# Optimization experiments

Measured on AMD Instinct MI355X. Metric: run time of the kernel, lower is better.

Reference implementation:

```python
import jax, jax.numpy as jnp
import numpy as np

DIM_V = 768
DIM_T = 768
HIDDEN = 256
MAX_KEEP = 96


def setup_inputs() -> dict:
    key = jax.random.key(0)
    k1, k2, k3, k4, k5 = jax.random.split(key, 5)
    B, N, S = 64, 1024, 64
    dense_visual = jax.random.normal(k1, (B, N, DIM_V), dtype=jnp.float32)
    text_embedding = jax.random.normal(k2, (B, S, DIM_T), dtype=jnp.float32)
    din = DIM_V + DIM_T
    # Linear params (stored as [in, out] for x @ W)
    W1 = jax.random.normal(k3, (din, HIDDEN), dtype=jnp.float32) / np.sqrt(din)
    b1 = jnp.zeros((HIDDEN,), dtype=jnp.float32)
    W2 = jax.random.normal(k4, (HIDDEN, 1), dtype=jnp.float32) / np.sqrt(HIDDEN)
    b2 = jnp.zeros((1,), dtype=jnp.float32)
    register_token = jax.random.normal(k5, (1, 1, DIM_V), dtype=jnp.float32) * 0.02
    return {
        "dense_visual": dense_visual,
        "text_embedding": text_embedding,
        "W1": W1, "b1": b1, "W2": W2, "b2": b2,
        "register_token": register_token,
    }


def reference(dense_visual, text_embedding, W1, b1, W2, b2, register_token):
    B, N, D = dense_visual.shape
    # Top-down context: mean-pooled text broadcast over patches
    ctx = jnp.broadcast_to(text_embedding.mean(axis=1, keepdims=True), (B, N, text_embedding.shape[-1]))
    scorer_in = jnp.concatenate([dense_visual, ctx], axis=-1)  # [B, N, 1536]
    h = jax.nn.relu(jnp.einsum('bnd,dh->bnh', scorer_in, W1) + b1)
    scores = jax.nn.sigmoid(jnp.einsum('bnh,ho->bno', h, W2) + b2).squeeze(-1)  # [B, N]
    num_keep = max(1, min(MAX_KEEP, N))
    _, top_k_idx = jax.lax.top_k(scores, num_keep)  # [B, K]
    top_k_idx = jnp.sort(top_k_idx, axis=1)
    sparse_visual = jnp.take_along_axis(dense_visual, top_k_idx[..., None], axis=1)  # [B, K, D]
    register = jnp.broadcast_to(register_token, (B, 1, D))
    final_visual = jnp.concatenate([sparse_visual, register], axis=1)  # [B, K+1, D]
    return final_visual, top_k_idx
```

## Files before the change

### kernel.cpp

```cpp
#include <hip/hip_runtime.h>
#include <hip/hip_bf16.h>

#define B_   64
#define N_   1024
#define S_   64
#define DV   768
#define DT   768
#define HID  256
#define KEEP 96

#define KB2  64
#define NKS2 (DV / KB2)
#define SCALE_A 32.0f
#define SCALE_W 32.0f
#define SCALE_LOGIT (SCALE_A * SCALE_W)

typedef _Float16 half8_t __attribute__((ext_vector_type(8)));
typedef float f32x4 __attribute__((ext_vector_type(4)));

__global__ __launch_bounds__(256) void pack_w_kernel(
    const float* __restrict__ W1, _Float16* __restrict__ Wh,
    _Float16* __restrict__ Wl) {
  int d = blockIdx.x;
  int h = threadIdx.x;
  float w = W1[d * HID + h] * SCALE_W;
  _Float16 hi = (_Float16)w;
  _Float16 lo = (_Float16)(w - (float)hi);
  int g = d >> 5, r = d & 31;
  int lane = ((r >> 3) << 4) | (h & 15);
  int i = r & 7, c = h >> 4;
  size_t off = ((size_t)((g * 16 + c) * 64 + lane)) * 8 + i;
  Wh[off] = hi;
  Wl[off] = lo;
}

__global__ __launch_bounds__(1024) void ctx_proj_kernel(
    const float* __restrict__ text,
    const float* __restrict__ W1,
    const float* __restrict__ b1,
    float* __restrict__ ctx_proj) {
  int b = blockIdx.x;
  int t = threadIdx.x;
  __shared__ float ctx[DT];
  __shared__ float red[4][HID];
  if (t < DT) {
    const float* p = text + (size_t)b * S_ * DT + t;
    float a0 = 0.f, a1 = 0.f, a2 = 0.f, a3 = 0.f;
    for (int s = 0; s < S_; s += 4) {
      a0 += p[(size_t)(s + 0) * DT];
      a1 += p[(size_t)(s + 1) * DT];
      a2 += p[(size_t)(s + 2) * DT];
      a3 += p[(size_t)(s + 3) * DT];
    }
    ctx[t] = ((a0 + a1) + (a2 + a3)) * (1.0f / S_);
  }
  __syncthreads();
  int p4 = t >> 8;
  int h  = t & 255;
  int db = p4 * 192;
  const float* wcol = W1 + (size_t)(DV + db) * HID + h;
  float s0 = 0.f, s1 = 0.f, s2 = 0.f, s3 = 0.f;
  #pragma unroll 4
  for (int d = 0; d < 192; d += 4) {
    s0 = fmaf(ctx[db + d + 0], wcol[(size_t)(d + 0) * HID], s0);
    s1 = fmaf(ctx[db + d + 1], wcol[(size_t)(d + 1) * HID], s1);
    s2 = fmaf(ctx[db + d + 2], wcol[(size_t)(d + 2) * HID], s2);
    s3 = fmaf(ctx[db + d + 3], wcol[(size_t)(d + 3) * HID], s3);
  }
  red[p4][h] = ((s0 + s1) + (s2 + s3));
  __syncthreads();
  if (t < HID)
    ctx_proj[b * HID + t] =
        SCALE_LOGIT * (b1[t] + ((red[0][t] + red[1][t]) + (red[2][t] + red[3][t])));
}

__device__ inline void cvt_split8(float4 a, float4 b, half8_t& hi, half8_t& lo) {
  float x[8] = {a.x, a.y, a.z, a.w, b.x, b.y, b.z, b.w};
  #pragma unroll
  for (int i = 0; i < 8; ++i) {
    float v = x[i] * SCALE_A;
    _Float16 h = (_Float16)v;
    hi[i] = h;
    lo[i] = (_Float16)(v - (float)h);
  }
}

__global__ __launch_bounds__(256, 2) void score_kernel(
    const float* __restrict__ A,
    const _Float16* __restrict__ WhP,
    const _Float16* __restrict__ WlP,
    const float* __restrict__ W2,
    const float* __restrict__ ctx_proj,
    float* __restrict__ logits) {
  __shared__ half8_t AhS[2][512];
  __shared__ half8_t AlS[2][512];
  __shared__ float red[64][4];

  const int t = threadIdx.x;
  const int lane = t & 63;
  const int w = t >> 6;
  const int r0 = blockIdx.x * 64;
  const int batch = r0 >> 10;

  const int arow = t >> 2;
  const int k0 = (t & 3) * 16;
  const float* aptr = A + (size_t)(r0 + arow) * DV + k0;
  const int ksub0 = k0 >> 5;
  const int kq0 = (k0 & 31) >> 3;
  const int dst1 = (ksub0 * 4 + kq0) * 64 + arow;
  const int dst2 = dst1 + 64;

  const half8_t* WhV = (const half8_t*)WhP;
  const half8_t* WlV = (const half8_t*)WlP;

  f32x4 acc[4][4];
  #pragma unroll
  for (int rt = 0; rt < 4; ++rt)
    #pragma unroll
    for (int j = 0; j < 4; ++j) acc[rt][j] = (f32x4){0.f, 0.f, 0.f, 0.f};

  {
    float4 v0 = *(const float4*)(aptr + 0);
    float4 v1 = *(const float4*)(aptr + 4);
    float4 v2 = *(const float4*)(aptr + 8);
    float4 v3 = *(const float4*)(aptr + 12);
    half8_t h0, l0, h1, l1;
    cvt_split8(v0, v1, h0, l0);
    cvt_split8(v2, v3, h1, l1);
    AhS[0][dst1] = h0; AlS[0][dst1] = l0;
    AhS[0][dst2] = h1; AlS[0][dst2] = l1;
  }
  __syncthreads();

  #pragma unroll 2
  for (int ks = 0; ks < NKS2; ++ks) {
    const int cur = ks & 1;
    float4 nv0, nv1, nv2, nv3;
    if (ks + 1 < NKS2) {
      const float* ap = aptr + (ks + 1) * KB2;
      nv0 = *(const float4*)(ap + 0);
      nv1 = *(const float4*)(ap + 4);
      nv2 = *(const float4*)(ap + 8);
      nv3 = *(const float4*)(ap + 12);
    }
    #pragma unroll
    for (int ksub = 0; ksub < 2; ++ksub) {
      half8_t bh[4], bl[4];
      #pragma unroll
      for (int j = 0; j < 4; ++j) {
        int bi = ((ks * 2 + ksub) * 16 + w * 4 + j) * 64 + lane;
        bh[j] = WhV[bi];
        bl[j] = WlV[bi];
      }
      half8_t ah[4], al[4];
      #pragma unroll
      for (int rt = 0; rt < 4; ++rt) {
        int ai = (ksub * 4 + (lane >> 4)) * 64 + rt * 16 + (lane & 15);
        ah[rt] = AhS[cur][ai];
        al[rt] = AlS[cur][ai];
      }
      #pragma unroll
      for (int rt = 0; rt < 4; ++rt)
        #pragma unroll
        for (int j = 0; j < 4; ++j) {
          acc[rt][j] = __builtin_amdgcn_mfma_f32_16x16x32_f16(ah[rt], bh[j], acc[rt][j], 0, 0, 0);
          acc[rt][j] = __builtin_amdgcn_mfma_f32_16x16x32_f16(ah[rt], bl[j], acc[rt][j], 0, 0, 0);
          acc[rt][j] = __builtin_amdgcn_mfma_f32_16x16x32_f16(al[rt], bh[j], acc[rt][j], 0, 0, 0);
        }
    }
    if (ks + 1 < NKS2) {
      half8_t h0, l0, h1, l1;
      cvt_split8(nv0, nv1, h0, l0);
      cvt_split8(nv2, nv3, h1, l1);
      AhS[cur ^ 1][dst1] = h0; AlS[cur ^ 1][dst1] = l0;
      AhS[cur ^ 1][dst2] = h1; AlS[cur ^ 1][dst2] = l1;
    }
    __syncthreads();
  }

  const int hbase = w * 64 + (lane & 15);
  const float* ctxp = ctx_proj + batch * HID;
  float psum[4][4];
  #pragma unroll
  for (int rt = 0; rt < 4; ++rt)
    #pragma unroll
    for (int r = 0; r < 4; ++r) psum[rt][r] = 0.f;
  #pragma unroll
  for (int j = 0; j < 4; ++j) {
    int hcol = hbase + j * 16;
    float cj = ctxp[hcol];
    float w2j = W2[hcol];
    #pragma unroll
    for (int rt = 0; rt < 4; ++rt)
      #pragma unroll
      for (int r = 0; r < 4; ++r)
        psum[rt][r] = fmaf(fmaxf(acc[rt][j][r] + cj, 0.f), w2j, psum[rt][r]);
  }
  #pragma unroll
  for (int m = 1; m < 16; m <<= 1)
    #pragma unroll
    for (int rt = 0; rt < 4; ++rt)
      #pragma unroll
      for (int r = 0; r < 4; ++r)
        psum[rt][r] += __shfl_xor(psum[rt][r], m, 64);
  if ((lane & 15) == 0) {
    int rowg = (lane >> 4) * 4;
    #pragma unroll
    for (int rt = 0; rt < 4; ++rt)
      #pragma unroll
      for (int r = 0; r < 4; ++r) red[rt * 16 + rowg + r][w] = psum[rt][r];
  }
  __syncthreads();
  if (t < 64) logits[r0 + t] = red[t][0] + red[t][1] + red[t][2] + red[t][3];
}

__global__ __launch_bounds__(1024) void topk_kernel(
    const float* __restrict__ logits,
    int* __restrict__ idx_ws,
    float* __restrict__ out,
    int out_idx_base) {
  int b = blockIdx.x;
  int t = threadIdx.x;
  __shared__ float s[N_];
  __shared__ int   si[N_];
  __shared__ int   t2[128];

  s[t]  = logits[b * N_ + t];
  si[t] = t;
  __syncthreads();

  for (int k = 2; k <= N_; k <<= 1) {
    for (int j = k >> 1; j > 0; j >>= 1) {
      int ixj = t ^ j;
      if (ixj > t) {
        float s1 = s[t], s2 = s[ixj];
        int   i1 = si[t], i2 = si[ixj];
        bool before = (s1 > s2) || (s1 == s2 && i1 < i2);
        bool doSwap = ((t & k) == 0) ? !before : before;
        if (doSwap) { s[t] = s2; s[ixj] = s1; si[t] = i2; si[ixj] = i1; }
      }
      __syncthreads();
    }
  }

  if (t < 128) t2[t] = (t < KEEP) ? si[t] : 0x7FFFFFFF;
  __syncthreads();
  for (int k = 2; k <= 128; k <<= 1) {
    for (int j = k >> 1; j > 0; j >>= 1) {
      if (t < 128) {
        int ixj = t ^ j;
        if (ixj > t) {
          int a = t2[t], c = t2[ixj];
          bool before = a < c;
          bool doSwap = ((t & k) == 0) ? !before : before;
          if (doSwap) { t2[t] = c; t2[ixj] = a; }
        }
      }
      __syncthreads();
    }
  }

  if (t < KEEP) {
    int v = t2[t];
    idx_ws[b * KEEP + t] = v;
    out[out_idx_base + b * KEEP + t] = (float)v;
  }
}

__global__ __launch_bounds__(192) void gather_kernel(
    const float* __restrict__ A,
    const float* __restrict__ reg_tok,
    const int* __restrict__ idx_ws,
    float* __restrict__ out) {
  int blk = blockIdx.x;
  int b = blk / (KEEP + 1), r = blk % (KEEP + 1);
  int t = threadIdx.x;
  const float* src;
  if (r == KEEP) {
    src = reg_tok;
  } else {
    int idx = idx_ws[b * KEEP + r];
    src = A + ((size_t)b * N_ + idx) * DV;
  }
  float4 v = *(const float4*)&src[t * 4];
  *(float4*)&out[((size_t)b * (KEEP + 1) + r) * DV + t * 4] = v;
}

extern "C" void kernel_launch(void* const* d_in, const int* in_sizes, int n_in,
                              void* d_out, int out_size, void* d_ws, size_t ws_size,
                              hipStream_t stream) {
  (void)in_sizes; (void)n_in; (void)out_size; (void)ws_size;
  const float* dense_visual = (const float*)d_in[0];
  const float* text_emb     = (const float*)d_in[1];
  const float* W1           = (const float*)d_in[2];
  const float* b1           = (const float*)d_in[3];
  const float* W2           = (const float*)d_in[4];
  const float* reg_tok      = (const float*)d_in[6];
  float* out = (float*)d_out;

  char* ws = (char*)d_ws;
  float*     ctx_proj = (float*)(ws + 0);
  float*     logits   = (float*)(ws + 65536);
  int*       idx_ws   = (int*)(ws + 327680);
  _Float16*  Wh       = (_Float16*)(ws + 352256);
  _Float16*  Wl       = (_Float16*)(ws + 745472);

  const int out_idx_base = B_ * (KEEP + 1) * DV;

  pack_w_kernel<<<DV, 256, 0, stream>>>(W1, Wh, Wl);
  ctx_proj_kernel<<<B_, 1024, 0, stream>>>(text_emb, W1, b1, ctx_proj);
  score_kernel<<<(B_ * N_) / 64, 256, 0, stream>>>(dense_visual, Wh, Wl, W2, ctx_proj, logits);
  topk_kernel<<<B_, 1024, 0, stream>>>(logits, idx_ws, out, out_idx_base);
  gather_kernel<<<B_ * (KEEP + 1), 192, 0, stream>>>(dense_visual, reg_tok, idx_ws, out);
}
```

Measured before the change: 378.7 us.

## Software-pipeline weight fragment loads across k-substeps and use lightweight LDS barrier

Restructures the score kernel's main loop so the global weight fragments for the next k-substep are prefetched into registers while MFMAs for the current substep run. The two ksub iterations are unrolled explicitly with double-buffered B registers, and the next A tile's LDS writes are moved between the two compute halves. __syncthreads is replaced with a custom barrier that waits only on LDS counters, so outstanding global loads no longer stall the barrier. In exchange, register pressure rises, which could cause spills at the 2-wave occupancy bound.

```diff
diff --git a/kernel.cpp b/kernel.cpp
--- a/kernel.cpp
+++ b/kernel.cpp
@@ -85,6 +85,13 @@
   }
 }
 
+__device__ inline void lds_barrier() {
+  asm volatile("s_waitcnt lgkmcnt(0)" ::: "memory");
+  __builtin_amdgcn_sched_barrier(0);
+  __builtin_amdgcn_s_barrier();
+  asm volatile("" ::: "memory");
+}
+
 __global__ __launch_bounds__(256, 2) void score_kernel(
     const float* __restrict__ A,
     const _Float16* __restrict__ WhP,
@@ -105,9 +112,7 @@
   const int arow = t >> 2;
   const int k0 = (t & 3) * 16;
   const float* aptr = A + (size_t)(r0 + arow) * DV + k0;
-  const int ksub0 = k0 >> 5;
-  const int kq0 = (k0 & 31) >> 3;
-  const int dst1 = (ksub0 * 4 + kq0) * 64 + arow;
+  const int dst1 = ((t & 3) * 2) * 64 + arow;
   const int dst2 = dst1 + 64;
 
   const half8_t* WhV = (const half8_t*)WhP;
@@ -118,6 +123,8 @@
   for (int rt = 0; rt < 4; ++rt)
     #pragma unroll
     for (int j = 0; j < 4; ++j) acc[rt][j] = (f32x4){0.f, 0.f, 0.f, 0.f};
+
+  half8_t bh0[4], bl0[4], bh1[4], bl1[4];
 
   {
     float4 v0 = *(const float4*)(aptr + 0);
@@ -130,32 +137,40 @@
     AhS[0][dst1] = h0; AlS[0][dst1] = l0;
     AhS[0][dst2] = h1; AlS[0][dst2] = l1;
   }
-  __syncthreads();
-
+  #pragma unroll
+  for (int j = 0; j < 4; ++j) {
+    int bi = (w * 4 + j) * 64 + lane;
+    bh0[j] = WhV[bi];
+    bl0[j] = WlV[bi];
+  }
+  lds_barrier();
+
+  float4 av0, av1, av2, av3;
   #pragma unroll 2
   for (int ks = 0; ks < NKS2; ++ks) {
     const int cur = ks & 1;
-    float4 nv0, nv1, nv2, nv3;
     if (ks + 1 < NKS2) {
       const float* ap = aptr + (ks + 1) * KB2;
-      nv0 = *(const float4*)(ap + 0);
-      nv1 = *(const float4*)(ap + 4);
-      nv2 = *(const float4*)(ap + 8);
-      nv3 = *(const float4*)(ap + 12);
-    }
-    #pragma unroll
-    for (int ksub = 0; ksub < 2; ++ksub) {
-      half8_t bh[4], bl[4];
+      av0 = *(const float4*)(ap + 0);
+      av1 = *(const float4*)(ap + 4);
+      av2 = *(const float4*)(ap + 8);
+      av3 = *(const float4*)(ap + 12);
+    }
+
+    {
+      const int g = 2 * ks + 1;
       #pragma unroll
       for (int j = 0; j < 4; ++j) {
-        int bi = ((ks * 2 + ksub) * 16 + w * 4 + j) * 64 + lane;
-        bh[j] = WhV[bi];
-        bl[j] = WlV[bi];
-      }
+        int bi = (g * 16 + w * 4 + j) * 64 + lane;
+        bh1[j] = WhV[bi];
+        bl1[j] = WlV[bi];
+      }
+    }
+    {
       half8_t ah[4], al[4];
       #pragma unroll
       for (int rt = 0; rt < 4; ++rt) {
-        int ai = (ksub * 4 + (lane >> 4)) * 64 + rt * 16 + (lane & 15);
+        int ai = (lane >> 4) * 64 + rt * 16 + (lane & 15);
         ah[rt] = AhS[cur][ai];
         al[rt] = AlS[cur][ai];
       }
@@ -163,19 +178,44 @@
       for (int rt = 0; rt < 4; ++rt)
         #pragma unroll
         for (int j = 0; j < 4; ++j) {
-          acc[rt][j] = __builtin_amdgcn_mfma_f32_16x16x32_f16(ah[rt], bh[j], acc[rt][j], 0, 0, 0);
-          acc[rt][j] = __builtin_amdgcn_mfma_f32_16x16x32_f16(ah[rt], bl[j], acc[rt][j], 0, 0, 0);
-          acc[rt][j] = __builtin_amdgcn_mfma_f32_16x16x32_f16(al[rt], bh[j], acc[rt][j], 0, 0, 0);
+          acc[rt][j] = __builtin_amdgcn_mfma_f32_16x16x32_f16(ah[rt], bh0[j], acc[rt][j], 0, 0, 0);
+          acc[rt][j] = __builtin_amdgcn_mfma_f32_16x16x32_f16(ah[rt], bl0[j], acc[rt][j], 0, 0, 0);
+          acc[rt][j] = __builtin_amdgcn_mfma_f32_16x16x32_f16(al[rt], bh0[j], acc[rt][j], 0, 0, 0);
         }
     }
+
     if (ks + 1 < NKS2) {
+      const int g = 2 * ks + 2;
+      #pragma unroll
+      for (int j = 0; j < 4; ++j) {
+        int bi = (g * 16 + w * 4 + j) * 64 + lane;
+        bh0[j] = WhV[bi];
+        bl0[j] = WlV[bi];
+      }
       half8_t h0, l0, h1, l1;
-      cvt_split8(nv0, nv1, h0, l0);
-      cvt_split8(nv2, nv3, h1, l1);
+      cvt_split8(av0, av1, h0, l0);
+      cvt_split8(av2, av3, h1, l1);
       AhS[cur ^ 1][dst1] = h0; AlS[cur ^ 1][dst1] = l0;
       AhS[cur ^ 1][dst2] = h1; AlS[cur ^ 1][dst2] = l1;
     }
-    __syncthreads();
+    {
+      half8_t ah[4], al[4];
+      #pragma unroll
+      for (int rt = 0; rt < 4; ++rt) {
+        int ai = (4 + (lane >> 4)) * 64 + rt * 16 + (lane & 15);
+        ah[rt] = AhS[cur][ai];
+        al[rt] = AlS[cur][ai];
+      }
+      #pragma unroll
+      for (int rt = 0; rt < 4; ++rt)
+        #pragma unroll
+        for (int j = 0; j < 4; ++j) {
+          acc[rt][j] = __builtin_amdgcn_mfma_f32_16x16x32_f16(ah[rt], bh1[j], acc[rt][j], 0, 0, 0);
+          acc[rt][j] = __builtin_amdgcn_mfma_f32_16x16x32_f16(ah[rt], bl1[j], acc[rt][j], 0, 0, 0);
+          acc[rt][j] = __builtin_amdgcn_mfma_f32_16x16x32_f16(al[rt], bh1[j], acc[rt][j], 0, 0, 0);
+        }
+    }
+    lds_barrier();
   }
 
   const int hbase = w * 64 + (lane & 15);
```

Result: faster. 361.8 us (-4.5%).
